# Optimization experiments

Hardware: AMD Instinct MI355X
Metric: run time of the kernel (lower is better)

The kernel has to match this reference:

```python
import jax, jax.numpy as jnp
import numpy as np

E = 2048   # embed_dim
H = 16     # num_heads
D = E // H # head_dim = 128
ROPE_BASE = 10000.0


def setup_inputs() -> dict:
    key = jax.random.key(0)
    ks = jax.random.split(key, 9)
    s = 0.02
    x = jax.random.normal(ks[0], (2, 2048, E), dtype=jnp.float32)
    Wq = jax.random.normal(ks[1], (E, E), dtype=jnp.float32) * s
    bq = jax.random.normal(ks[2], (E,), dtype=jnp.float32) * s
    Wk = jax.random.normal(ks[3], (E, E), dtype=jnp.float32) * s
    bk = jax.random.normal(ks[4], (E,), dtype=jnp.float32) * s
    Wv = jax.random.normal(ks[5], (E, E), dtype=jnp.float32) * s
    bv = jax.random.normal(ks[6], (E,), dtype=jnp.float32) * s
    Wo = jax.random.normal(ks[7], (E, E), dtype=jnp.float32) * s
    bo = jax.random.normal(ks[8], (E,), dtype=jnp.float32) * s
    return {"x": x, "Wq": Wq, "bq": bq, "Wk": Wk, "bk": bk,
            "Wv": Wv, "bv": bv, "Wo": Wo, "bo": bo}


def _rope_cos_sin(seq_len, dtype):
    inv_freq = 1.0 / (ROPE_BASE ** (jnp.arange(0, D, 2, dtype=jnp.float32) / D))
    pos = jnp.arange(seq_len, dtype=jnp.float32)
    freqs = pos[:, None] * inv_freq[None, :]          # (S, D/2)
    emb = jnp.concatenate([freqs, freqs], axis=-1)    # (S, D)
    return jnp.cos(emb).astype(dtype), jnp.sin(emb).astype(dtype)


def _rotate_half(t):
    t1, t2 = jnp.split(t, 2, axis=-1)
    return jnp.concatenate([-t2, t1], axis=-1)


def reference(x, Wq, bq, Wk, bk, Wv, bv, Wo, bo):
    B, S, _ = x.shape
    # QKV projections (torch Linear: x @ W.T + b)
    q = (x @ Wq.T + bq).reshape(B, S, H, D).transpose(0, 2, 1, 3)  # (B,H,S,D)
    k = (x @ Wk.T + bk).reshape(B, S, H, D).transpose(0, 2, 1, 3)
    v = (x @ Wv.T + bv).reshape(B, S, H, D).transpose(0, 2, 1, 3)
    # RoPE
    cos, sin = _rope_cos_sin(S, x.dtype)              # (S, D) each
    q = q * cos + _rotate_half(q) * sin
    k = k * cos + _rotate_half(k) * sin
    # Causal scaled dot-product attention
    scale = 1.0 / jnp.sqrt(jnp.asarray(D, dtype=x.dtype))
    scores = jnp.einsum('bhqd,bhkd->bhqk', q, k) * scale
    causal = jnp.tril(jnp.ones((S, S), dtype=bool))
    scores = jnp.where(causal, scores, jnp.asarray(-jnp.inf, dtype=x.dtype))
    attn = jax.nn.softmax(scores, axis=-1)
    out = jnp.einsum('bhqk,bhkd->bhqd', attn, v)      # (B,H,S,D)
    out = out.transpose(0, 2, 1, 3).reshape(B, S, E)
    return out @ Wo.T + bo
```

## Files before the change

### kernel.cpp

```cpp
#include <hip/hip_runtime.h>
#include <math.h>

typedef __bf16 bf16;
typedef __attribute__((ext_vector_type(2))) __bf16 bf16x2;
typedef __attribute__((ext_vector_type(4))) __bf16 bf16x4;
typedef __attribute__((ext_vector_type(8))) __bf16 bf16x8;
typedef __attribute__((ext_vector_type(4))) float f32x4;

#define GLD16(g, l) __builtin_amdgcn_global_load_lds( \
    (const __attribute__((address_space(1))) void*)(g), \
    (__attribute__((address_space(3))) void*)(l), 16, 0, 0)

template<int N> __device__ __forceinline__ void wait_vm() {
  static_assert(N == 0 || N == 4 || N == 6, "");
  if constexpr (N == 0) asm volatile("s_waitcnt vmcnt(0)" ::: "memory");
  else if constexpr (N == 4) asm volatile("s_waitcnt vmcnt(4)" ::: "memory");
  else asm volatile("s_waitcnt vmcnt(6)" ::: "memory");
}

__global__ void prep_kernel(const float* __restrict__ x,
                            const float* __restrict__ Wq, const float* __restrict__ Wk,
                            const float* __restrict__ Wv, const float* __restrict__ Wo,
                            const float* __restrict__ bq, const float* __restrict__ bk,
                            const float* __restrict__ bv,
                            bf16* __restrict__ xb, bf16* __restrict__ wqkv, bf16* __restrict__ wob,
                            float* __restrict__ biasq, float* __restrict__ cost, float* __restrict__ sint) {
  const int bid = blockIdx.x, t = threadIdx.x;
  if (bid < 24576) {
    const float* src;
    bf16* dst;
    int i;
    if (bid < 8192)       { src = x;  dst = xb;                    i = bid * 256 + t; }
    else if (bid < 12288) { src = Wq; dst = wqkv;                  i = (bid - 8192) * 256 + t; }
    else if (bid < 16384) { src = Wk; dst = wqkv + 2048 * 2048;    i = (bid - 12288) * 256 + t; }
    else if (bid < 20480) { src = Wv; dst = wqkv + 2 * 2048 * 2048; i = (bid - 16384) * 256 + t; }
    else                  { src = Wo; dst = wob;                   i = (bid - 20480) * 256 + t; }
    float4 f = ((const float4*)src)[i];
    bf16x4 o;
    o[0] = (bf16)f.x; o[1] = (bf16)f.y; o[2] = (bf16)f.z; o[3] = (bf16)f.w;
    ((bf16x4*)dst)[i] = o;
  } else if (bid < 25088) {
    int i = (bid - 24576) * 256 + t;
    int s = i >> 6, d = i & 63;
    float inv = powf(10000.0f, -(float)d / 64.0f);
    float ang = (float)s * inv;
    cost[i] = cosf(ang);
    sint[i] = sinf(ang);
  } else {
    int i = (bid - 25088) * 256 + t;
    biasq[i] = (i < 2048) ? bq[i] : (i < 4096 ? bk[i - 2048] : bv[i - 4096]);
  }
}

__global__ void rope_tv_kernel(const bf16* __restrict__ qkv,
                               const float* __restrict__ cost, const float* __restrict__ sint,
                               bf16* __restrict__ kr, bf16* __restrict__ vt) {
  __shared__ bf16 Vl[64 * 72];
  const int t = threadIdx.x;
  if (blockIdx.x < 4096) {
    int idx = blockIdx.x * 256 + t;
    int dp = idx & 15;
    int h = (idx >> 4) & 15;
    int s = (idx >> 8) & 2047;
    int b = idx >> 19;
    int d0 = dp * 4;
    const bf16* row = qkv + ((size_t)(b * 2048 + s) * 6144) + 2048 + h * 128;
    bf16x4 klo = *(const bf16x4*)&row[d0];
    bf16x4 khi = *(const bf16x4*)&row[d0 + 64];
    float4 c4 = *(const float4*)&cost[(s << 6) + d0];
    float4 s4 = *(const float4*)&sint[(s << 6) + d0];
    float cf[4] = {c4.x, c4.y, c4.z, c4.w};
    float sf[4] = {s4.x, s4.y, s4.z, s4.w};
    bf16x4 olo, ohi;
#pragma unroll
    for (int j = 0; j < 4; ++j) {
      float kl = (float)klo[j], kh = (float)khi[j];
      olo[j] = (bf16)(kl * cf[j] - kh * sf[j]);
      ohi[j] = (bf16)(kh * cf[j] + kl * sf[j]);
    }
    bf16* orow = kr + (((size_t)(b * 16 + h) * 2048 + s) * 128);
    *(bf16x4*)&orow[d0] = olo;
    *(bf16x4*)&orow[d0 + 64] = ohi;
  } else {
    int vbid = blockIdx.x - 4096;
    const int dt = vbid & 1, st = (vbid >> 1) & 31, bh = vbid >> 6;
    const int b = bh >> 4, h = bh & 15;
    const bf16* src = qkv + ((size_t)(b * 2048 + st * 64) * 6144) + 4096 + h * 128 + dt * 64;
    bf16* dst = vt + ((size_t)bh * 128 + dt * 64) * 2048 + st * 64;
#pragma unroll
    for (int i = 0; i < 2; ++i) {
      int c = i * 256 + t;
      int r = c >> 3, c0 = (c & 7) * 8;
      *(bf16x8*)&Vl[r * 72 + c0] = *(const bf16x8*)&src[(size_t)r * 6144 + c0];
    }
    __syncthreads();
#pragma unroll
    for (int i = 0; i < 2; ++i) {
      int c = i * 256 + t;
      int r = c >> 3, c0 = (c & 7) * 8;
      bf16x8 v;
#pragma unroll
      for (int j = 0; j < 8; ++j) v[j] = Vl[(c0 + j) * 72 + r];
      *(bf16x8*)&dst[(size_t)r * 2048 + c0] = v;
    }
  }
}

template<int BN, bool OUT_BF16>
__global__ __launch_bounds__(256, 2)
void gemm4w_kernel(const bf16* __restrict__ A, const bf16* __restrict__ B,
                   const float* __restrict__ bias, void* __restrict__ Cp,
                   int M, int N, int K) {
  constexpr int NB = BN / 64;
  constexpr int NR = BN / 32;
  __shared__ bf16 Al[2][128 * 64];
  __shared__ bf16 Bl[2][NB][64 * 64];
  const int t = threadIdx.x;
  const int wid = t >> 6, lane = t & 63;
  const int wr = wid >> 1, wc = wid & 1;
  const int lr = lane & 15, lk = lane >> 4;
  const int flat = (int)blockIdx.x;
  const int xcd = flat & 7, r0 = flat >> 3;
  const int tm = xcd * 4 + (r0 & 3);
  const int tn = r0 >> 2;
  const bf16* Ab = A + (size_t)tm * 128 * K;
  const bf16* Bb = B + (size_t)tn * BN * K;
  const int NT = K >> 6;

  auto stageA = [&](int bp, int h, int kt) {
#pragma unroll
    for (int q = 0; q < 2; ++q) {
      int e = q * 256 + t;
      int r = e >> 3, c = e & 7;
      GLD16(Ab + (size_t)(h * 64 + r) * K + kt * 64 + ((c ^ (r & 7)) << 3),
            &Al[bp][h * 4096 + e * 8]);
    }
  };
  auto stageB = [&](int bp, int unit, int kt) {
#pragma unroll
    for (int q = 0; q < 2; ++q) {
      int e = q * 256 + t;
      int r = e >> 3, c = e & 7;
      GLD16(Bb + (size_t)(unit * 64 + r) * K + kt * 64 + ((c ^ (r & 7)) << 3),
            &Bl[bp][unit][e * 8]);
    }
  };
  auto readA = [&](int bp, int m, int kk) -> bf16x8 {
    int row = wr * 64 + m * 16 + lr;
    return *(const bf16x8*)&Al[bp][row * 64 + ((((kk << 2) | lk) ^ (row & 7)) << 3)];
  };
  auto readB = [&](int bp, int n, int kk) -> bf16x8 {
    int rb = wc * (NR * 16) + n * 16 + lr;
    return *(const bf16x8*)&Bl[bp][rb >> 6][(rb & 63) * 64 + ((((kk << 2) | lk) ^ (rb & 7)) << 3)];
  };

  f32x4 acc[4][NR] = {};

#pragma unroll
  for (int un = 0; un < NB; ++un) stageB(0, un, 0);
  stageA(0, 0, 0); stageA(0, 1, 0);
  if (NT > 1) {
#pragma unroll
    for (int un = 0; un < NB; ++un) stageB(1, un, 1);
    wait_vm<2 * NB>();
  } else {
    wait_vm<0>();
  }
  __builtin_amdgcn_s_barrier();
  __builtin_amdgcn_sched_barrier(0);

  for (int u = 0; u < NT; ++u) {
    const int p = u & 1;
    bf16x8 bfr[NR][2], afr[4];
#pragma unroll
    for (int n = 0; n < NR; ++n)
#pragma unroll
      for (int kk = 0; kk < 2; ++kk) bfr[n][kk] = readB(p, n, kk);
#pragma unroll
    for (int m = 0; m < 4; ++m) afr[m] = readA(p, m, 0);
    if (u + 1 < NT) { stageA(p ^ 1, 0, u + 1); stageA(p ^ 1, 1, u + 1); }
    __builtin_amdgcn_s_barrier();
    asm volatile("s_waitcnt lgkmcnt(0)" ::: "memory");
    __builtin_amdgcn_sched_barrier(0);
    __builtin_amdgcn_s_setprio(1);
#pragma unroll
    for (int m = 0; m < 4; ++m)
#pragma unroll
      for (int n = 0; n < NR; ++n)
        acc[m][n] = __builtin_amdgcn_mfma_f32_16x16x32_bf16(afr[m], bfr[n][0], acc[m][n], 0, 0, 0);
    __builtin_amdgcn_s_setprio(0);
    __builtin_amdgcn_sched_barrier(0);
#pragma unroll
    for (int m = 0; m < 4; ++m) afr[m] = readA(p, m, 1);
    if (u + 2 < NT) {
#pragma unroll
      for (int un = 0; un < NB; ++un) stageB(p, un, u + 2);
    }
    __builtin_amdgcn_s_barrier();
    asm volatile("s_waitcnt lgkmcnt(0)" ::: "memory");
    __builtin_amdgcn_sched_barrier(0);
    __builtin_amdgcn_s_setprio(1);
#pragma unroll
    for (int m = 0; m < 4; ++m)
#pragma unroll
      for (int n = 0; n < NR; ++n)
        acc[m][n] = __builtin_amdgcn_mfma_f32_16x16x32_bf16(afr[m], bfr[n][1], acc[m][n], 0, 0, 0);
    __builtin_amdgcn_s_setprio(0);
    __builtin_amdgcn_sched_barrier(0);
    if (u + 2 < NT) { wait_vm<2 * NB>(); }
    else            { wait_vm<0>(); }
    __builtin_amdgcn_s_barrier();
    __builtin_amdgcn_sched_barrier(0);
  }

  const int rbase = tm * 128 + wr * 64, cbase = tn * BN + wc * (NR * 16);
#pragma unroll
  for (int n = 0; n < NR; ++n) {
    int col = cbase + n * 16 + lr;
    float bvl = bias[col];
#pragma unroll
    for (int m = 0; m < 4; ++m) {
#pragma unroll
      for (int rr = 0; rr < 4; ++rr) {
        int row = rbase + m * 16 + lk * 4 + rr;
        float v = acc[m][n][rr] + bvl;
        if (OUT_BF16) ((bf16*)Cp)[(size_t)row * N + col] = (bf16)v;
        else          ((float*)Cp)[(size_t)row * N + col] = v;
      }
    }
  }
}

__global__ __launch_bounds__(256, 3)
void attn_kernel(const bf16* __restrict__ qkv, const bf16* __restrict__ Kc,
                 const bf16* __restrict__ Vtg, const float* __restrict__ cost,
                 const float* __restrict__ sint, bf16* __restrict__ O, int S) {
  __shared__ bf16 Kl[2][64 * 128];
  __shared__ bf16 Vt[2][128 * 64];
  __shared__ bf16 Pl[4][16 * 64];
  const int t = threadIdx.x, wid = t >> 6, lane = t & 63;
  const int lr = lane & 15, lk = lane >> 4;
  const int flat = (int)blockIdx.x;
  const int xcd = flat & 7, kk2 = flat >> 3;
  const int bh = xcd * 4 + (kk2 >> 4);
  const int b = bh >> 4, h = bh & 15;
  const int NQ = S >> 6;
  const int qtA = kk2 & 15, qtB = NQ - 1 - qtA;
  const int ntA = qtA + 1, ntB = qtB + 1, total = ntA + ntB;
  const bf16* Kb = Kc + (size_t)bh * S * 128;
  const bf16* Vb = Vtg + (size_t)bh * 128 * S;
  const float SCL2 = 0.12752040147f;

  bf16x8 qf[4];
  auto loadQ = [&](int q0) {
    int qrow = q0 + wid * 16 + lr;
    const bf16* qp = qkv + (size_t)(b * 2048 + qrow) * 6144 + h * 128;
    bf16x8 raw[4];
#pragma unroll
    for (int kb = 0; kb < 4; ++kb) raw[kb] = *(const bf16x8*)&qp[kb * 32 + lk * 8];
#pragma unroll
    for (int kb = 0; kb < 4; ++kb) {
      const float* cb = cost + (qrow << 6) + ((kb & 1) << 5) + lk * 8;
      const float* sb = sint + (qrow << 6) + ((kb & 1) << 5) + lk * 8;
#pragma unroll
      for (int j = 0; j < 8; ++j) {
        float qv = (float)raw[kb][j];
        float qo = (float)raw[kb ^ 2][j];
        float rot = (kb < 2) ? -qo : qo;
        qf[kb][j] = (bf16)((qv * cb[j] + rot * sb[j]) * SCL2);
      }
    }
  };
  auto stage = [&](int buf, int kv0) {
#pragma unroll
    for (int c = 0; c < 4; ++c) {
      int fc = c * 256 + t;
      int kvr = fc >> 4, cc = fc & 15;
      GLD16(Kb + (size_t)(kv0 + kvr) * 128 + (cc ^ (kvr & 7)) * 8, &Kl[buf][fc * 8]);
      int dr = fc >> 3, c2 = fc & 7;
      GLD16(Vb + (size_t)dr * S + kv0 + (c2 ^ (dr & 7)) * 8, &Vt[buf][fc * 8]);
    }
  };

  f32x4 o[8] = {};
  float mrun[4], lrun[4];
#pragma unroll
  for (int r = 0; r < 4; ++r) { mrun[r] = -INFINITY; lrun[r] = 0.f; }

  loadQ(qtA * 64);
  stage(0, 0);
  __syncthreads();
  int cur = 0;
  for (int ti = 0; ti < total; ++ti) {
    if (ti + 1 < total) {
      int tn = ti + 1;
      stage(cur ^ 1, ((tn < ntA) ? tn : tn - ntA) * 64);
    }
    __builtin_amdgcn_sched_barrier(0);
    const bool isA = ti < ntA;
    const int tt = isA ? ti : ti - ntA;
    const int nt = isA ? ntA : ntB;
    const int q0 = (isA ? qtA : qtB) * 64;
    const int kv0 = tt * 64;
    f32x4 sa[4];
    __builtin_amdgcn_s_setprio(1);
#pragma unroll
    for (int n = 0; n < 4; ++n) {
      sa[n] = (f32x4){0.f, 0.f, 0.f, 0.f};
      int kvl = n * 16 + lr;
#pragma unroll
      for (int kb = 0; kb < 4; ++kb) {
        bf16x8 kf = *(const bf16x8*)&Kl[cur][kvl * 128 + (((kb << 2) | lk) ^ (kvl & 7)) * 8];
        sa[n] = __builtin_amdgcn_mfma_f32_16x16x32_bf16(qf[kb], kf, sa[n], 0, 0, 0);
      }
    }
    __builtin_amdgcn_s_setprio(0);
    float p[4][4];
    float tmax[4] = {-INFINITY, -INFINITY, -INFINITY, -INFINITY};
    const bool lastTile = (tt == nt - 1);
#pragma unroll
    for (int n = 0; n < 4; ++n)
#pragma unroll
      for (int r = 0; r < 4; ++r) {
        float s = sa[n][r];
        if (lastTile) {
          int kvg = kv0 + n * 16 + lr;
          int qg = q0 + wid * 16 + lk * 4 + r;
          if (kvg > qg) s = -INFINITY;
        }
        p[n][r] = s;
        tmax[r] = fmaxf(tmax[r], s);
      }
    bool need = false;
#pragma unroll
    for (int r = 0; r < 4; ++r) need = need || (tmax[r] > mrun[r] + 6.0f);
    if (__any(need)) {
#pragma unroll
      for (int r = 0; r < 4; ++r) {
#pragma unroll
        for (int off = 1; off < 16; off <<= 1)
          tmax[r] = fmaxf(tmax[r], __shfl_xor(tmax[r], off));
        float mnew = fmaxf(mrun[r], tmax[r]);
        float alpha = exp2f(mrun[r] - mnew);
        mrun[r] = mnew;
        lrun[r] *= alpha;
#pragma unroll
        for (int n8 = 0; n8 < 8; ++n8) o[n8][r] *= alpha;
      }
    }
#pragma unroll
    for (int n = 0; n < 4; ++n)
#pragma unroll
      for (int r = 0; r < 4; ++r)
        p[n][r] = exp2f(p[n][r] - mrun[r]);
#pragma unroll
    for (int n = 0; n < 4; ++n)
#pragma unroll
      for (int r = 0; r < 4; ++r) {
        int row = lk * 4 + r, col = n * 16 + lr;
        Pl[wid][(row * 64 + col) ^ ((row & 7) << 3)] = (bf16)p[n][r];
      }
    __builtin_amdgcn_s_setprio(1);
#pragma unroll
    for (int kb2 = 0; kb2 < 2; ++kb2) {
      bf16x8 pf = *(const bf16x8*)&Pl[wid][(lr * 64 + kb2 * 32 + lk * 8) ^ ((lr & 7) << 3)];
#pragma unroll
      for (int n8 = 0; n8 < 8; ++n8) {
        int dcol = n8 * 16 + lr;
        bf16x8 vf = *(const bf16x8*)&Vt[cur][(dcol * 64 + kb2 * 32 + lk * 8) ^ ((dcol & 7) << 3)];
        o[n8] = __builtin_amdgcn_mfma_f32_16x16x32_bf16(pf, vf, o[n8], 0, 0, 0);
      }
    }
    __builtin_amdgcn_s_setprio(0);
    {
      float rsum[4];
#pragma unroll
      for (int r = 0; r < 4; ++r) {
        rsum[r] = (p[0][r] + p[1][r]) + (p[2][r] + p[3][r]);
#pragma unroll
        for (int off = 1; off < 16; off <<= 1)
          rsum[r] += __shfl_xor(rsum[r], off);
        lrun[r] += rsum[r];
      }
    }
    if (ti == ntA - 1) {
#pragma unroll
      for (int r = 0; r < 4; ++r) {
        float rl = 1.0f / lrun[r];
        int row = qtA * 64 + wid * 16 + lk * 4 + r;
        size_t base = ((size_t)(b * S + row)) * 2048 + h * 128;
#pragma unroll
        for (int n8 = 0; n8 < 8; ++n8)
          O[base + n8 * 16 + lr] = (bf16)(o[n8][r] * rl);
      }
#pragma unroll
      for (int n8 = 0; n8 < 8; ++n8) o[n8] = (f32x4){0.f, 0.f, 0.f, 0.f};
#pragma unroll
      for (int r = 0; r < 4; ++r) { mrun[r] = -INFINITY; lrun[r] = 0.f; }
      loadQ(qtB * 64);
    }
    __syncthreads();
    cur ^= 1;
  }
#pragma unroll
  for (int r = 0; r < 4; ++r) {
    float rl = 1.0f / lrun[r];
    int row = qtB * 64 + wid * 16 + lk * 4 + r;
    size_t base = ((size_t)(b * S + row)) * 2048 + h * 128;
#pragma unroll
    for (int n8 = 0; n8 < 8; ++n8)
      O[base + n8 * 16 + lr] = (bf16)(o[n8][r] * rl);
  }
}


extern "C" void kernel_launch(void* const* d_in, const int* in_sizes, int n_in,
                              void* d_out, int out_size, void* d_ws, size_t ws_size,
                              hipStream_t stream) {
  const float* x  = (const float*)d_in[0];
  const float* Wq = (const float*)d_in[1];
  const float* bq = (const float*)d_in[2];
  const float* Wk = (const float*)d_in[3];
  const float* bk = (const float*)d_in[4];
  const float* Wv = (const float*)d_in[5];
  const float* bv = (const float*)d_in[6];
  const float* Wo = (const float*)d_in[7];
  const float* bo = (const float*)d_in[8];

  char* ws = (char*)d_ws;
  bf16* xb     = (bf16*)(ws);
  bf16* wqkv   = (bf16*)(ws + 16777216);
  bf16* wob    = (bf16*)(ws + 41943040);
  bf16* qkv    = (bf16*)(ws + 50331648);
  bf16* kr     = (bf16*)(ws + 100663296);
  bf16* vt     = (bf16*)(ws + 117440512);
  float* biasq = (float*)(ws + 134217728);
  float* cost  = (float*)(ws + 134242304);
  float* sint  = (float*)(ws + 134766592);
  bf16* attn_out = xb;

  prep_kernel<<<25112, 256, 0, stream>>>(x, Wq, Wk, Wv, Wo, bq, bk, bv,
                                         xb, wqkv, wob, biasq, cost, sint);
  gemm4w_kernel<192, true><<<1024, 256, 0, stream>>>(xb, wqkv, biasq, qkv, 4096, 6144, 2048);
  rope_tv_kernel<<<6144, 256, 0, stream>>>(qkv, cost, sint, kr, vt);
  attn_kernel<<<512, 256, 0, stream>>>(qkv, kr, vt, cost, sint, attn_out, 2048);
  gemm4w_kernel<128, false><<<512, 256, 0, stream>>>(attn_out, wob, bo, (float*)d_out, 4096, 2048, 2048);
}
```

Measured before the change: 268.3 us.

## Process both causal query tiles concurrently in 8-wave blocks sharing K/V tiles

The attention kernel now launches 512-thread blocks where waves 0-3 handle query tile A and waves 4-7 handle the paired tile B at the same time. Previously one 4-wave block walked tile A and then tile B in sequence. Each staged K/V tile is now loaded once and used by both halves, which removes the duplicate K/V reloads and the serial sweep, and each thread issues half as many staging copies. Tile pairing is also reordered so each XCD gets a mix of short and long pairs. The cost is that tile-A waves sit idle at barriers while tile B finishes its longer range, and higher per-block LDS and register pressure may reduce occupancy.

New measurement: 488.2 us. +82.0%, slower.

```diff
diff --git a/kernel.cpp b/kernel.cpp
--- a/kernel.cpp
+++ b/kernel.cpp
@@ -231,29 +231,31 @@
   }
 }
 
-__global__ __launch_bounds__(256, 3)
+__global__ __launch_bounds__(512, 4)
 void attn_kernel(const bf16* __restrict__ qkv, const bf16* __restrict__ Kc,
                  const bf16* __restrict__ Vtg, const float* __restrict__ cost,
                  const float* __restrict__ sint, bf16* __restrict__ O, int S) {
   __shared__ bf16 Kl[2][64 * 128];
   __shared__ bf16 Vt[2][128 * 64];
-  __shared__ bf16 Pl[4][16 * 64];
+  __shared__ bf16 Pl[8][16 * 64];
   const int t = threadIdx.x, wid = t >> 6, lane = t & 63;
   const int lr = lane & 15, lk = lane >> 4;
   const int flat = (int)blockIdx.x;
   const int xcd = flat & 7, kk2 = flat >> 3;
   const int bh = xcd * 4 + (kk2 >> 4);
   const int b = bh >> 4, h = bh & 15;
-  const int NQ = S >> 6;
-  const int qtA = kk2 & 15, qtB = NQ - 1 - qtA;
-  const int ntA = qtA + 1, ntB = qtB + 1, total = ntA + ntB;
+  const int j = kk2 & 15;
+  const int qtA = (j & 1) ? (15 - (j >> 1)) : (j >> 1);
+  const int qtB = 31 - qtA;
+  const int qt = (wid < 4) ? qtA : qtB;
+  const int wg = wid & 3;
   const bf16* Kb = Kc + (size_t)bh * S * 128;
   const bf16* Vb = Vtg + (size_t)bh * 128 * S;
   const float SCL2 = 0.12752040147f;
 
   bf16x8 qf[4];
-  auto loadQ = [&](int q0) {
-    int qrow = q0 + wid * 16 + lr;
+  {
+    int qrow = qt * 64 + wg * 16 + lr;
     const bf16* qp = qkv + (size_t)(b * 2048 + qrow) * 6144 + h * 128;
     bf16x8 raw[4];
 #pragma unroll
@@ -263,18 +265,18 @@
       const float* cb = cost + (qrow << 6) + ((kb & 1) << 5) + lk * 8;
       const float* sb = sint + (qrow << 6) + ((kb & 1) << 5) + lk * 8;
 #pragma unroll
-      for (int j = 0; j < 8; ++j) {
-        float qv = (float)raw[kb][j];
-        float qo = (float)raw[kb ^ 2][j];
+      for (int jj = 0; jj < 8; ++jj) {
+        float qv = (float)raw[kb][jj];
+        float qo = (float)raw[kb ^ 2][jj];
         float rot = (kb < 2) ? -qo : qo;
-        qf[kb][j] = (bf16)((qv * cb[j] + rot * sb[j]) * SCL2);
-      }
-    }
-  };
+        qf[kb][jj] = (bf16)((qv * cb[jj] + rot * sb[jj]) * SCL2);
+      }
+    }
+  }
   auto stage = [&](int buf, int kv0) {
 #pragma unroll
-    for (int c = 0; c < 4; ++c) {
-      int fc = c * 256 + t;
+    for (int c = 0; c < 2; ++c) {
+      int fc = c * 512 + t;
       int kvr = fc >> 4, cc = fc & 15;
       GLD16(Kb + (size_t)(kv0 + kvr) * 128 + (cc ^ (kvr & 7)) * 8, &Kl[buf][fc * 8]);
       int dr = fc >> 3, c2 = fc & 7;
@@ -287,129 +289,109 @@
 #pragma unroll
   for (int r = 0; r < 4; ++r) { mrun[r] = -INFINITY; lrun[r] = 0.f; }
 
-  loadQ(qtA * 64);
   stage(0, 0);
   __syncthreads();
   int cur = 0;
-  for (int ti = 0; ti < total; ++ti) {
-    if (ti + 1 < total) {
-      int tn = ti + 1;
-      stage(cur ^ 1, ((tn < ntA) ? tn : tn - ntA) * 64);
-    }
-    __builtin_amdgcn_sched_barrier(0);
-    const bool isA = ti < ntA;
-    const int tt = isA ? ti : ti - ntA;
-    const int nt = isA ? ntA : ntB;
-    const int q0 = (isA ? qtA : qtB) * 64;
-    const int kv0 = tt * 64;
-    f32x4 sa[4];
-    __builtin_amdgcn_s_setprio(1);
-#pragma unroll
-    for (int n = 0; n < 4; ++n) {
-      sa[n] = (f32x4){0.f, 0.f, 0.f, 0.f};
-      int kvl = n * 16 + lr;
-#pragma unroll
-      for (int kb = 0; kb < 4; ++kb) {
-        bf16x8 kf = *(const bf16x8*)&Kl[cur][kvl * 128 + (((kb << 2) | lk) ^ (kvl & 7)) * 8];
-        sa[n] = __builtin_amdgcn_mfma_f32_16x16x32_bf16(qf[kb], kf, sa[n], 0, 0, 0);
-      }
-    }
-    __builtin_amdgcn_s_setprio(0);
-    float p[4][4];
-    float tmax[4] = {-INFINITY, -INFINITY, -INFINITY, -INFINITY};
-    const bool lastTile = (tt == nt - 1);
-#pragma unroll
-    for (int n = 0; n < 4; ++n)
-#pragma unroll
-      for (int r = 0; r < 4; ++r) {
-        float s = sa[n][r];
-        if (lastTile) {
-          int kvg = kv0 + n * 16 + lr;
-          int qg = q0 + wid * 16 + lk * 4 + r;
-          if (kvg > qg) s = -INFINITY;
-        }
-        p[n][r] = s;
-        tmax[r] = fmaxf(tmax[r], s);
-      }
-    bool need = false;
-#pragma unroll
-    for (int r = 0; r < 4; ++r) need = need || (tmax[r] > mrun[r] + 6.0f);
-    if (__any(need)) {
-#pragma unroll
-      for (int r = 0; r < 4; ++r) {
-#pragma unroll
-        for (int off = 1; off < 16; off <<= 1)
-          tmax[r] = fmaxf(tmax[r], __shfl_xor(tmax[r], off));
-        float mnew = fmaxf(mrun[r], tmax[r]);
-        float alpha = exp2f(mrun[r] - mnew);
-        mrun[r] = mnew;
-        lrun[r] *= alpha;
-#pragma unroll
-        for (int n8 = 0; n8 < 8; ++n8) o[n8][r] *= alpha;
-      }
-    }
-#pragma unroll
-    for (int n = 0; n < 4; ++n)
-#pragma unroll
-      for (int r = 0; r < 4; ++r)
-        p[n][r] = exp2f(p[n][r] - mrun[r]);
-#pragma unroll
-    for (int n = 0; n < 4; ++n)
-#pragma unroll
-      for (int r = 0; r < 4; ++r) {
-        int row = lk * 4 + r, col = n * 16 + lr;
-        Pl[wid][(row * 64 + col) ^ ((row & 7) << 3)] = (bf16)p[n][r];
-      }
-    __builtin_amdgcn_s_setprio(1);
-#pragma unroll
-    for (int kb2 = 0; kb2 < 2; ++kb2) {
-      bf16x8 pf = *(const bf16x8*)&Pl[wid][(lr * 64 + kb2 * 32 + lk * 8) ^ ((lr & 7) << 3)];
-#pragma unroll
-      for (int n8 = 0; n8 < 8; ++n8) {
-        int dcol = n8 * 16 + lr;
-        bf16x8 vf = *(const bf16x8*)&Vt[cur][(dcol * 64 + kb2 * 32 + lk * 8) ^ ((dcol & 7) << 3)];
-        o[n8] = __builtin_amdgcn_mfma_f32_16x16x32_bf16(pf, vf, o[n8], 0, 0, 0);
-      }
-    }
-    __builtin_amdgcn_s_setprio(0);
-    {
-      float rsum[4];
-#pragma unroll
-      for (int r = 0; r < 4; ++r) {
-        rsum[r] = (p[0][r] + p[1][r]) + (p[2][r] + p[3][r]);
-#pragma unroll
-        for (int off = 1; off < 16; off <<= 1)
-          rsum[r] += __shfl_xor(rsum[r], off);
-        lrun[r] += rsum[r];
-      }
-    }
-    if (ti == ntA - 1) {
-#pragma unroll
-      for (int r = 0; r < 4; ++r) {
-        float rl = 1.0f / lrun[r];
-        int row = qtA * 64 + wid * 16 + lk * 4 + r;
-        size_t base = ((size_t)(b * S + row)) * 2048 + h * 128;
-#pragma unroll
-        for (int n8 = 0; n8 < 8; ++n8)
-          O[base + n8 * 16 + lr] = (bf16)(o[n8][r] * rl);
-      }
-#pragma unroll
-      for (int n8 = 0; n8 < 8; ++n8) o[n8] = (f32x4){0.f, 0.f, 0.f, 0.f};
-#pragma unroll
-      for (int r = 0; r < 4; ++r) { mrun[r] = -INFINITY; lrun[r] = 0.f; }
-      loadQ(qtB * 64);
+  for (int tt = 0; tt <= qtB; ++tt) {
+    if (tt < qtB) stage(cur ^ 1, (tt + 1) * 64);
+    __builtin_amdgcn_sched_barrier(0);
+    if (tt <= qt) {
+      const int kv0 = tt * 64;
+      f32x4 sa[4];
+      __builtin_amdgcn_s_setprio(1);
+#pragma unroll
+      for (int n = 0; n < 4; ++n) {
+        sa[n] = (f32x4){0.f, 0.f, 0.f, 0.f};
+        int kvl = n * 16 + lr;
+#pragma unroll
+        for (int kb = 0; kb < 4; ++kb) {
+          bf16x8 kf = *(const bf16x8*)&Kl[cur][kvl * 128 + (((kb << 2) | lk) ^ (kvl & 7)) * 8];
+          sa[n] = __builtin_amdgcn_mfma_f32_16x16x32_bf16(qf[kb], kf, sa[n], 0, 0, 0);
+        }
+      }
+      __builtin_amdgcn_s_setprio(0);
+      float p[4][4];
+      float tmax[4] = {-INFINITY, -INFINITY, -INFINITY, -INFINITY};
+      const bool lastTile = (tt == qt);
+#pragma unroll
+      for (int n = 0; n < 4; ++n)
+#pragma unroll
+        for (int r = 0; r < 4; ++r) {
+          float s = sa[n][r];
+          if (lastTile) {
+            int kvg = kv0 + n * 16 + lr;
+            int qg = qt * 64 + wg * 16 + lk * 4 + r;
+            if (kvg > qg) s = -INFINITY;
+          }
+          p[n][r] = s;
+          tmax[r] = fmaxf(tmax[r], s);
+        }
+      bool need = false;
+#pragma unroll
+      for (int r = 0; r < 4; ++r) need = need || (tmax[r] > mrun[r] + 6.0f);
+      if (__any(need)) {
+#pragma unroll
+        for (int r = 0; r < 4; ++r) {
+#pragma unroll
+          for (int off = 1; off < 16; off <<= 1)
+            tmax[r] = fmaxf(tmax[r], __shfl_xor(tmax[r], off));
+          float mnew = fmaxf(mrun[r], tmax[r]);
+          float alpha = exp2f(mrun[r] - mnew);
+          mrun[r] = mnew;
+          lrun[r] *= alpha;
+#pragma unroll
+          for (int n8 = 0; n8 < 8; ++n8) o[n8][r] *= alpha;
+        }
+      }
+#pragma unroll
+      for (int n = 0; n < 4; ++n)
+#pragma unroll
+        for (int r = 0; r < 4; ++r)
+          p[n][r] = exp2f(p[n][r] - mrun[r]);
+#pragma unroll
+      for (int n = 0; n < 4; ++n)
+#pragma unroll
+        for (int r = 0; r < 4; ++r) {
+          int row = lk * 4 + r, col = n * 16 + lr;
+          Pl[wid][(row * 64 + col) ^ ((row & 7) << 3)] = (bf16)p[n][r];
+        }
+      __builtin_amdgcn_s_setprio(1);
+#pragma unroll
+      for (int kb2 = 0; kb2 < 2; ++kb2) {
+        bf16x8 pf = *(const bf16x8*)&Pl[wid][(lr * 64 + kb2 * 32 + lk * 8) ^ ((lr & 7) << 3)];
+#pragma unroll
+        for (int n8 = 0; n8 < 8; ++n8) {
+          int dcol = n8 * 16 + lr;
+          bf16x8 vf = *(const bf16x8*)&Vt[cur][(dcol * 64 + kb2 * 32 + lk * 8) ^ ((dcol & 7) << 3)];
+          o[n8] = __builtin_amdgcn_mfma_f32_16x16x32_bf16(pf, vf, o[n8], 0, 0, 0);
+        }
+      }
+      __builtin_amdgcn_s_setprio(0);
+      {
+        float rsum[4];
+#pragma unroll
+        for (int r = 0; r < 4; ++r) {
+          rsum[r] = (p[0][r] + p[1][r]) + (p[2][r] + p[3][r]);
+#pragma unroll
+          for (int off = 1; off < 16; off <<= 1)
+            rsum[r] += __shfl_xor(rsum[r], off);
+          lrun[r] += rsum[r];
+        }
+      }
+      if (lastTile) {
+#pragma unroll
+        for (int r = 0; r < 4; ++r) {
+          float rl = 1.0f / lrun[r];
+          int row = qt * 64 + wg * 16 + lk * 4 + r;
+          size_t base = ((size_t)(b * S + row)) * 2048 + h * 128;
+#pragma unroll
+          for (int n8 = 0; n8 < 8; ++n8)
+            O[base + n8 * 16 + lr] = (bf16)(o[n8][r] * rl);
+        }
+      }
     }
     __syncthreads();
     cur ^= 1;
-  }
-#pragma unroll
-  for (int r = 0; r < 4; ++r) {
-    float rl = 1.0f / lrun[r];
-    int row = qtB * 64 + wid * 16 + lk * 4 + r;
-    size_t base = ((size_t)(b * S + row)) * 2048 + h * 128;
-#pragma unroll
-    for (int n8 = 0; n8 < 8; ++n8)
-      O[base + n8 * 16 + lr] = (bf16)(o[n8][r] * rl);
   }
 }
 
@@ -443,6 +425,6 @@
                                          xb, wqkv, wob, biasq, cost, sint);
   gemm4w_kernel<192, true><<<1024, 256, 0, stream>>>(xb, wqkv, biasq, qkv, 4096, 6144, 2048);
   rope_tv_kernel<<<6144, 256, 0, stream>>>(qkv, cost, sint, kr, vt);
-  attn_kernel<<<512, 256, 0, stream>>>(qkv, kr, vt, cost, sint, attn_out, 2048);
+  attn_kernel<<<512, 512, 0, stream>>>(qkv, kr, vt, cost, sint, attn_out, 2048);
   gemm4w_kernel<128, false><<<512, 256, 0, stream>>>(attn_out, wob, bo, (float*)d_out, 4096, 2048, 2048);
 }
```
